# Kernel optimization log

Hardware: AMD Instinct MI355X
Metric: run time of the kernel (lower is better)

## Reference

```python
import jax, jax.numpy as jnp
import numpy as np
from jax import lax

B_, K_, T_, V_ = 2, 4, 1024, 1024
D_MODEL, EXPAND = 512, 2
D_INNER = EXPAND * D_MODEL          # 1024
N_STATE, D_CONV, DT_RANK, L_ = 16, 4, 32, 2


def setup_inputs() -> dict:
    key = jax.random.key(0)
    ks = jax.random.split(key, 9)
    s = 0.02
    A0 = jnp.log(jnp.arange(1, N_STATE + 1, dtype=jnp.float32))  # S4D-real init
    return {
        'codes': jax.random.randint(ks[0], (B_, K_, T_), 0, V_),
        'embed_w': jax.random.normal(ks[1], (K_, V_, D_MODEL), jnp.float32) * s,
        'norm_w': jnp.ones((L_, D_MODEL), jnp.float32),
        'in_proj_w': jax.random.normal(ks[2], (L_, 2 * D_INNER, D_MODEL), jnp.float32) * s,
        'conv_w': jax.random.normal(ks[3], (L_, D_INNER, 1, D_CONV), jnp.float32) * s,
        'conv_b': jnp.zeros((L_, D_INNER), jnp.float32),
        'x_proj_w': jax.random.normal(ks[4], (L_, DT_RANK + 2 * N_STATE, D_INNER), jnp.float32) * s,
        'dt_proj_w': jax.random.normal(ks[5], (L_, D_INNER, DT_RANK), jnp.float32) * s,
        'dt_proj_b': jnp.zeros((L_, D_INNER), jnp.float32),
        'A_log': jnp.broadcast_to(A0, (L_, D_INNER, N_STATE)) + 0.0,
        'D_skip': jnp.ones((L_, D_INNER), jnp.float32),
        'out_proj_w': jax.random.normal(ks[6], (L_, D_MODEL, D_INNER), jnp.float32) * s,
        'head_w': jax.random.normal(ks[7], (K_, D_MODEL, V_), jnp.float32) * s,
    }


def rmsnorm(x, w, eps=1e-6):
    return x * w * lax.rsqrt(jnp.mean(x * x, axis=-1, keepdims=True) + eps)


def causal_dwconv(x, w, b):
    # x: (B,T,D); w: (D,1,d_conv) depthwise; torch pads d_conv-1 both sides then slices [:T]
    # == left-pad-only causal conv.
    xt = x.transpose(0, 2, 1)  # (B,D,T)
    y = lax.conv_general_dilated(xt, w, (1,), [(D_CONV - 1, 0)],
                                 feature_group_count=D_INNER,
                                 dimension_numbers=('NCH', 'OIH', 'NCH'))
    return (y + b[None, :, None]).transpose(0, 2, 1)


def mamba_block(x, norm_w, in_w, cw, cb, xp_w, dtp_w, dtp_b, A_log, D_skip, out_w):
    res = x
    x = rmsnorm(x, norm_w)
    xz = x @ in_w.T                                   # (B,T,2*d_inner)
    x_ssm, z = jnp.split(xz, 2, axis=-1)
    x_ssm = jax.nn.silu(causal_dwconv(x_ssm, cw, cb))  # (B,T,D)
    x_dbl = x_ssm @ xp_w.T                            # (B,T,dt_rank+2N)
    dt_lr, Bm, Cm = jnp.split(x_dbl, [DT_RANK, DT_RANK + N_STATE], axis=-1)
    dt = jax.nn.softplus(dt_lr @ dtp_w.T + dtp_b)     # (B,T,D)
    A = -jnp.exp(A_log)                               # (D,N)
    dA = jnp.exp(dt[..., None] * A)                   # (B,T,D,N)
    dBx = dt[..., None] * Bm[:, :, None, :] * x_ssm[..., None]  # (B,T,D,N)

    def step(h, inp):
        dA_t, dBx_t, C_t = inp
        h = dA_t * h + dBx_t                          # (B,D,N)
        return h, jnp.einsum('bdn,bn->bd', h, C_t)

    h0 = jnp.zeros((x.shape[0], D_INNER, N_STATE), x.dtype)
    _, ys = lax.scan(step, h0, (dA.transpose(1, 0, 2, 3),
                                dBx.transpose(1, 0, 2, 3),
                                Cm.transpose(1, 0, 2)))
    y = ys.transpose(1, 0, 2) + x_ssm * D_skip        # (B,T,D)
    y = y * jax.nn.silu(z)
    return res + y @ out_w.T


def reference(codes, embed_w, norm_w, in_proj_w, conv_w, conv_b, x_proj_w,
              dt_proj_w, dt_proj_b, A_log, D_skip, out_proj_w, head_w):
    k_idx = jnp.arange(K_)[None, :, None]
    x = embed_w[k_idx, codes].sum(axis=1)             # (B,T,d_model): RVQ sum-embedding
    for l in range(L_):
        x = mamba_block(x, norm_w[l], in_proj_w[l], conv_w[l], conv_b[l],
                        x_proj_w[l], dt_proj_w[l], dt_proj_b[l],
                        A_log[l], D_skip[l], out_proj_w[l])
    return jnp.einsum('btd,kdv->bktv', x, head_w)     # (B,K,T,V)
```

## Files before the change

### kernel.cpp

```cpp
#include <hip/hip_runtime.h>
#include <hip/hip_bf16.h>


#define B_SZ 2
#define K_CB 4
#define T_SZ 1024
#define V_SZ 1024
#define DM 512
#define DI 1024
#define NS 16
#define DTR 32
#define NCHUNK 64
#define TCHUNK 16

typedef unsigned short u16;
typedef long long ll;
using short8 = __attribute__((ext_vector_type(8))) short;
using f32x4  = __attribute__((ext_vector_type(4))) float;

__device__ __forceinline__ float bf2f(u16 u) {
    union { unsigned int i; float f; } v; v.i = ((unsigned int)u) << 16; return v.f;
}
__device__ __forceinline__ u16 f2bf(float f) {
    union { float f; unsigned int i; } v; v.f = f;
    unsigned int x = v.i;
    return (u16)((x + 0x7fffu + ((x >> 16) & 1u)) >> 16);
}
__device__ __forceinline__ float siluf(float x) { return x / (1.f + __expf(-x)); }
__device__ __forceinline__ float softplusf(float x) { return (x > 20.f) ? x : log1pf(__expf(x)); }

__global__ __launch_bounds__(256) void mega0_k(const float* __restrict__ in_w,
                                               const float* __restrict__ xp_w,
                                               const float* __restrict__ dtp_w,
                                               const float* __restrict__ out_w,
                                               u16* __restrict__ w_in, u16* __restrict__ w_xp,
                                               u16* __restrict__ w_dt, u16* __restrict__ w_out,
                                               const float* __restrict__ head_w,
                                               u16* __restrict__ w_hd,
                                               const int* __restrict__ codes,
                                               const float* __restrict__ ew,
                                               const float* __restrict__ nw,
                                               float* __restrict__ x,
                                               u16* __restrict__ xn) {
    __shared__ float tile[64][65];
    int bid = blockIdx.x;
    int tid = threadIdx.x;
    if (bid < 3264) {
        int i = (bid * 256 + tid) << 2;
        const float* s; u16* d;
        if (i < 2097152) { s = in_w + i; d = w_in + i; }
        else {
            i -= 2097152;
            if (i < 131072) { s = xp_w + i; d = w_xp + i; }
            else {
                i -= 131072;
                if (i < 65536) { s = dtp_w + i; d = w_dt + i; }
                else { i -= 65536; s = out_w + i; d = w_out + i; }
            }
        }
        float4 v = *(const float4*)s;
        ushort4 o; o.x = f2bf(v.x); o.y = f2bf(v.y); o.z = f2bf(v.z); o.w = f2bf(v.w);
        *(ushort4*)d = o;
    } else if (bid < 3776) {
        int idx = bid - 3264;
        int z = idx >> 7, rest = idx & 127;
        int d0 = (rest >> 4) << 6, v0 = (rest & 15) << 6;
        int col = tid & 63, rbase = tid >> 6;
#pragma unroll
        for (int i = 0; i < 16; i++) {
            int row = (i << 2) + rbase;
            tile[row][col] = head_w[(ll)z * (DM * V_SZ) + (ll)(d0 + row) * V_SZ + v0 + col];
        }
        __syncthreads();
#pragma unroll
        for (int i = 0; i < 16; i++) {
            int vrow = (i << 2) + rbase;
            w_hd[(ll)z * (V_SZ * DM) + (ll)(v0 + vrow) * DM + d0 + col] = f2bf(tile[col][vrow]);
        }
    } else {
        int row = bid - 3776;
        int b = row >> 10, t = row & 1023;
        float a0 = 0.f, a1 = 0.f;
#pragma unroll
        for (int k = 0; k < K_CB; k++) {
            int c = codes[b * (K_CB * T_SZ) + k * T_SZ + t];
            a0 += ew[((ll)k * V_SZ + c) * DM + tid];
            a1 += ew[((ll)k * V_SZ + c) * DM + tid + 256];
        }
        x[(ll)row * DM + tid]       = a0;
        x[(ll)row * DM + tid + 256] = a1;
        float ss = a0 * a0 + a1 * a1;
#pragma unroll
        for (int off = 32; off > 0; off >>= 1) ss += __shfl_down(ss, off, 64);
        float* red = &tile[0][0];
        if ((tid & 63) == 0) red[tid >> 6] = ss;
        __syncthreads();
        float tot = red[0] + red[1] + red[2] + red[3];
        float scale = rsqrtf(tot * (1.0f / DM) + 1e-6f);
        xn[(ll)row * DM + tid]       = f2bf(a0 * scale * nw[tid]);
        xn[(ll)row * DM + tid + 256] = f2bf(a1 * scale * nw[tid + 256]);
    }
}

__global__ __launch_bounds__(256) void rmsnorm_k(const float* __restrict__ x,
                                                 const float* __restrict__ w,
                                                 u16* __restrict__ xn) {
    ll row = blockIdx.x;
    const float* xr = x + row * DM;
    int tid = threadIdx.x;
    float v0 = xr[tid], v1 = xr[tid + 256];
    float ss = v0 * v0 + v1 * v1;
#pragma unroll
    for (int off = 32; off > 0; off >>= 1) ss += __shfl_down(ss, off, 64);
    __shared__ float red[4];
    if ((tid & 63) == 0) red[tid >> 6] = ss;
    __syncthreads();
    float tot = red[0] + red[1] + red[2] + red[3];
    float scale = rsqrtf(tot * (1.0f / DM) + 1e-6f);
    xn[row * DM + tid]       = f2bf(v0 * scale * w[tid]);
    xn[row * DM + tid + 256] = f2bf(v1 * scale * w[tid + 256]);
}

template <int EP>
__global__ __launch_bounds__(256) void mgemm2_k(const u16* __restrict__ A, int lda,
                                                const u16* __restrict__ W,
                                                float* __restrict__ C,
                                                u16* __restrict__ Cb, int ldcb, int K) {
    __shared__ u16 As[2][4096];
    __shared__ u16 Bs[2][4096];
    int tid = threadIdx.x;
    int wave = tid >> 6, lane = tid & 63;
    int q = lane >> 4, r = lane & 15;
    int m0 = blockIdx.y << 7, n0 = blockIdx.x << 7;
    int wm = (wave >> 1) << 6, wn = (wave & 1) << 6;
    int srow = tid >> 1, soff = (tid & 1) << 4;
    const u16* Ap = A + (ll)(m0 + srow) * lda + soff;
    const u16* Wp = W + (ll)(n0 + srow) * K + soff;
    int sidx = (srow << 5) + soff;
    f32x4 acc[4][4];
#pragma unroll
    for (int i = 0; i < 4; i++)
#pragma unroll
        for (int j = 0; j < 4; j++) acc[i][j] = (f32x4){0.f, 0.f, 0.f, 0.f};

    uint4 ra0 = *(const uint4*)Ap,       ra1 = *(const uint4*)(Ap + 8);
    uint4 rb0 = *(const uint4*)Wp,       rb1 = *(const uint4*)(Wp + 8);
    *(uint4*)&As[0][sidx] = ra0; *(uint4*)&As[0][sidx + 8] = ra1;
    *(uint4*)&Bs[0][sidx] = rb0; *(uint4*)&Bs[0][sidx + 8] = rb1;
    __syncthreads();

    int p = 0;
    for (int k0 = 0; k0 < K; k0 += 32) {
        bool pf = (k0 + 32) < K;
        if (pf) {
            ra0 = *(const uint4*)(Ap + k0 + 32); ra1 = *(const uint4*)(Ap + k0 + 40);
            rb0 = *(const uint4*)(Wp + k0 + 32); rb1 = *(const uint4*)(Wp + k0 + 40);
        }
        short8 af[4], bfr[4];
#pragma unroll
        for (int i = 0; i < 4; i++) af[i]  = *(const short8*)&As[p][((wm + (i << 4) + r) << 5) + (q << 3)];
#pragma unroll
        for (int j = 0; j < 4; j++) bfr[j] = *(const short8*)&Bs[p][((wn + (j << 4) + r) << 5) + (q << 3)];
#pragma unroll
        for (int i = 0; i < 4; i++)
#pragma unroll
            for (int j = 0; j < 4; j++)
                acc[i][j] = __builtin_amdgcn_mfma_f32_16x16x32_bf16(af[i], bfr[j], acc[i][j], 0, 0, 0);
        if (pf) {
            *(uint4*)&As[p ^ 1][sidx] = ra0; *(uint4*)&As[p ^ 1][sidx + 8] = ra1;
            *(uint4*)&Bs[p ^ 1][sidx] = rb0; *(uint4*)&Bs[p ^ 1][sidx + 8] = rb1;
        }
        __syncthreads();
        p ^= 1;
    }

#pragma unroll
    for (int i = 0; i < 4; i++)
#pragma unroll
        for (int j = 0; j < 4; j++)
#pragma unroll
            for (int g = 0; g < 4; g++) {
                int m = m0 + wm + (i << 4) + (q << 2) + g;
                int n = n0 + wn + (j << 4) + r;
                float v = acc[i][j][g];
                if (EP == 0) {
                    Cb[(ll)m * ldcb + n] = f2bf(v);
                } else {
                    int z = n >> 10, vv = n & 1023;
                    int b = m >> 10, t = m & 1023;
                    C[((ll)(b * K_CB + z) * T_SZ + t) * V_SZ + vv] = v;
                }
            }
}

template <int EP>
__global__ __launch_bounds__(256) void mgemm_k(const u16* __restrict__ A, int lda,
                                               const u16* __restrict__ W,
                                               float* __restrict__ C, int ldc, int K,
                                               const float* __restrict__ bias,
                                               u16* __restrict__ Cb, int ldcb) {
    __shared__ u16 As[2][2048];
    __shared__ u16 Bs[2][2048];
    int tid = threadIdx.x;
    int m0 = blockIdx.y << 6, n0 = blockIdx.x << 6;
    int lane = tid & 63, wave = tid >> 6;
    int q = lane >> 4, r = lane & 15;
    int wm = (wave >> 1) << 5, wn = (wave & 1) << 5;
    int srow = tid >> 2, soff = (tid & 3) << 3;
    const u16* Ap = A + (ll)(m0 + srow) * lda + soff;
    const u16* Wp = W + (ll)(n0 + srow) * K + soff;
    int sidx = (srow << 5) + soff;
    f32x4 acc[2][2];
#pragma unroll
    for (int i = 0; i < 2; i++)
#pragma unroll
        for (int j = 0; j < 2; j++) acc[i][j] = (f32x4){0.f, 0.f, 0.f, 0.f};

    uint4 ra = *(const uint4*)Ap;
    uint4 rb = *(const uint4*)Wp;
    *(uint4*)&As[0][sidx] = ra;
    *(uint4*)&Bs[0][sidx] = rb;
    __syncthreads();

    int p = 0;
    for (int k0 = 0; k0 < K; k0 += 32) {
        bool pf = (k0 + 32) < K;
        if (pf) {
            ra = *(const uint4*)(Ap + k0 + 32);
            rb = *(const uint4*)(Wp + k0 + 32);
        }
        short8 af[2], bfr[2];
#pragma unroll
        for (int i = 0; i < 2; i++) af[i]  = *(const short8*)&As[p][((wm + (i << 4) + r) << 5) + (q << 3)];
#pragma unroll
        for (int j = 0; j < 2; j++) bfr[j] = *(const short8*)&Bs[p][((wn + (j << 4) + r) << 5) + (q << 3)];
#pragma unroll
        for (int i = 0; i < 2; i++)
#pragma unroll
            for (int j = 0; j < 2; j++)
                acc[i][j] = __builtin_amdgcn_mfma_f32_16x16x32_bf16(af[i], bfr[j], acc[i][j], 0, 0, 0);
        if (pf) {
            *(uint4*)&As[p ^ 1][sidx] = ra;
            *(uint4*)&Bs[p ^ 1][sidx] = rb;
        }
        __syncthreads();
        p ^= 1;
    }

#pragma unroll
    for (int i = 0; i < 2; i++)
#pragma unroll
        for (int j = 0; j < 2; j++)
#pragma unroll
            for (int g = 0; g < 4; g++) {
                int m = m0 + wm + (i << 4) + (q << 2) + g;
                int n = n0 + wn + (j << 4) + r;
                float v = acc[i][j][g];
                float nv = C[(ll)m * ldc + n] + v;
                C[(ll)m * ldc + n] = nv;
                Cb[(ll)m * ldcb + n] = f2bf(nv);
            }
}

__global__ __launch_bounds__(256) void convxp_k(const u16* __restrict__ xzb,
                                                const float* __restrict__ cw,
                                                const float* __restrict__ cb,
                                                const u16* __restrict__ W,
                                                float* __restrict__ xc,
                                                float* __restrict__ xdbl,
                                                u16* __restrict__ xdbl_bf) {
    __shared__ u16 xcs[16][1032];
    __shared__ u16 Bs[2][2048];
    int blk = blockIdx.x, tid = threadIdx.x;
    int b = blk >> 6, tg = blk & 63;
    int t0 = tg << 4;
    ll ro0 = (ll)b * T_SZ + t0;
    int c0 = tid << 2;
    float4 a = *(const float4*)&cb[c0];
    float4 cwv[4];
#pragma unroll
    for (int e = 0; e < 4; e++) cwv[e] = *(const float4*)&cw[(c0 + e) << 2];
    ushort4 v[19];
#pragma unroll
    for (int i = 0; i < 19; i++) {
        int t = t0 - 3 + i;
        if (t >= 0) v[i] = *(const ushort4*)&xzb[((ll)(b * T_SZ + t)) * (2 * DI) + c0];
        else        v[i] = (ushort4){0, 0, 0, 0};
    }
#pragma unroll
    for (int tr = 0; tr < 16; tr++) {
        float acc0 = a.x, acc1 = a.y, acc2 = a.z, acc3 = a.w;
#pragma unroll
        for (int j = 0; j < 4; j++) {
            ushort4 vv = v[tr + j];
            acc0 = fmaf(bf2f(vv.x), ((const float*)&cwv[0])[j], acc0);
            acc1 = fmaf(bf2f(vv.y), ((const float*)&cwv[1])[j], acc1);
            acc2 = fmaf(bf2f(vv.z), ((const float*)&cwv[2])[j], acc2);
            acc3 = fmaf(bf2f(vv.w), ((const float*)&cwv[3])[j], acc3);
        }
        float4 s; ushort4 sb;
        s.x = siluf(acc0); s.y = siluf(acc1); s.z = siluf(acc2); s.w = siluf(acc3);
        sb.x = f2bf(s.x); sb.y = f2bf(s.y); sb.z = f2bf(s.z); sb.w = f2bf(s.w);
        *(float4*)&xc[(ro0 + tr) * DI + c0] = s;
        *(ushort4*)&xcs[tr][c0] = sb;
    }
    __syncthreads();

    int lane = tid & 63, wave = tid >> 6;
    int q = lane >> 4, r = lane & 15;
    int srow = tid >> 2, soff = (tid & 3) << 3;
    f32x4 acc = (f32x4){0.f, 0.f, 0.f, 0.f};
    uint4 rb = *(const uint4*)(W + (ll)srow * DI + soff);
    *(uint4*)&Bs[0][(srow << 5) + soff] = rb;
    __syncthreads();
    int p = 0;
    for (int k0 = 0; k0 < DI; k0 += 32) {
        bool pf = (k0 + 32) < DI;
        if (pf) rb = *(const uint4*)(W + (ll)srow * DI + k0 + 32 + soff);
        short8 af  = *(const short8*)&xcs[r][k0 + (q << 3)];
        short8 bfr = *(const short8*)&Bs[p][(((wave << 4) + r) << 5) + (q << 3)];
        acc = __builtin_amdgcn_mfma_f32_16x16x32_bf16(af, bfr, acc, 0, 0, 0);
        if (pf) *(uint4*)&Bs[p ^ 1][(srow << 5) + soff] = rb;
        __syncthreads();
        p ^= 1;
    }
#pragma unroll
    for (int g = 0; g < 4; g++) {
        int tr = (q << 2) + g;
        int n = (wave << 4) + r;
        float vv = acc[g];
        xdbl[(ro0 + tr) * 64 + n]    = vv;
        xdbl_bf[(ro0 + tr) * 64 + n] = f2bf(vv);
    }
}

__global__ __launch_bounds__(256) void dtscan1_k(const u16* __restrict__ A,
                                                 const u16* __restrict__ W,
                                                 const float* __restrict__ bias,
                                                 const float* __restrict__ xc,
                                                 const float* __restrict__ xdbl,
                                                 const float* __restrict__ A_log,
                                                 float* __restrict__ dtb,
                                                 float* __restrict__ pA,
                                                 float* __restrict__ U) {
    __shared__ u16 As[2048];
    __shared__ u16 Bs[2048];
    __shared__ float dts[64][65];
    __shared__ float BCs[64][16];
    __shared__ float xcs[64][65];
    int tid = threadIdx.x;
    int m0 = blockIdx.y << 6, n0 = blockIdx.x << 6;
    int lane = tid & 63, wave = tid >> 6;
    int q = lane >> 4, r = lane & 15;
    int wm = (wave >> 1) << 5, wn = (wave & 1) << 5;

    int xr = tid >> 2, xcb = (tid & 3) << 4;
    const float* xp = &xc[(ll)(m0 + xr) * DI + n0 + xcb];
    float4 xv0 = *(const float4*)(xp);
    float4 xv1 = *(const float4*)(xp + 4);
    float4 xv2 = *(const float4*)(xp + 8);
    float4 xv3 = *(const float4*)(xp + 12);

    {
        int srow = tid >> 2, soff = (tid & 3) << 3;
        *(uint4*)&As[(srow << 5) + soff] = *(const uint4*)(A + (ll)(m0 + srow) * 64 + soff);
        *(uint4*)&Bs[(srow << 5) + soff] = *(const uint4*)(W + (ll)(n0 + srow) * DTR + soff);
        int rr = tid >> 2, cc = (tid & 3) << 2;
        *(float4*)&BCs[rr][cc] = *(const float4*)&xdbl[(ll)(m0 + rr) * 64 + DTR + cc];
    }
    int sd = lane;
    int sc = wave;
    int dg = n0 + sd;
    float Av[NS];
#pragma unroll
    for (int n4 = 0; n4 < 4; n4++) {
        float4 alv = *(const float4*)&A_log[dg * NS + (n4 << 2)];
        Av[(n4 << 2) + 0] = -__expf(alv.x); Av[(n4 << 2) + 1] = -__expf(alv.y);
        Av[(n4 << 2) + 2] = -__expf(alv.z); Av[(n4 << 2) + 3] = -__expf(alv.w);
    }
    *(float4*)&xcs[xr][xcb]      = xv0;
    *(float4*)&xcs[xr][xcb + 4]  = xv1;
    *(float4*)&xcs[xr][xcb + 8]  = xv2;
    *(float4*)&xcs[xr][xcb + 12] = xv3;
    __syncthreads();

    f32x4 acc[2][2];
#pragma unroll
    for (int i = 0; i < 2; i++)
#pragma unroll
        for (int j = 0; j < 2; j++) acc[i][j] = (f32x4){0.f, 0.f, 0.f, 0.f};
    short8 af[2], bfr[2];
#pragma unroll
    for (int i = 0; i < 2; i++) af[i]  = *(const short8*)&As[((wm + (i << 4) + r) << 5) + (q << 3)];
#pragma unroll
    for (int j = 0; j < 2; j++) bfr[j] = *(const short8*)&Bs[((wn + (j << 4) + r) << 5) + (q << 3)];
#pragma unroll
    for (int i = 0; i < 2; i++)
#pragma unroll
        for (int j = 0; j < 2; j++)
            acc[i][j] = __builtin_amdgcn_mfma_f32_16x16x32_bf16(af[i], bfr[j], acc[i][j], 0, 0, 0);

#pragma unroll
    for (int i = 0; i < 2; i++)
#pragma unroll
        for (int j = 0; j < 2; j++)
#pragma unroll
            for (int g = 0; g < 4; g++) {
                int mm = wm + (i << 4) + (q << 2) + g;
                int nn = wn + (j << 4) + r;
                float dtl = softplusf(acc[i][j][g] + bias[n0 + nn]);
                dtb[(ll)(m0 + mm) * DI + (n0 + nn)] = dtl;
                dts[mm][nn] = dtl;
            }
    __syncthreads();

    int b = m0 >> 10;
    int c = ((m0 & 1023) >> 4) + sc;
    int tl0 = sc << 4;
    float p[NS], u[NS];
#pragma unroll
    for (int n = 0; n < NS; n++) { p[n] = 1.f; u[n] = 0.f; }
#pragma unroll
    for (int s = 0; s < TCHUNK; s++) {
        int tl = tl0 + s;
        float dtv = dts[tl][sd];
        float xl = xcs[tl][sd];
        float dx = dtv * xl;
#pragma unroll
        for (int n = 0; n < NS; n++) {
            float aa = __expf(dtv * Av[n]);
            p[n] *= aa;
            u[n] = fmaf(aa, u[n], dx * BCs[tl][n]);
        }
    }
    ll o = ((ll)b * NCHUNK + c) * (NS * DI) + dg;
#pragma unroll
    for (int n = 0; n < NS; n++) { pA[o + n * DI] = p[n]; U[o + n * DI] = u[n]; }
}

__global__ __launch_bounds__(256) void scan2_k(const float* __restrict__ pA,
                                               const float* __restrict__ U,
                                               float* __restrict__ hst) {
    int i = blockIdx.x * 256 + threadIdx.x;
    int b = i >> 14;
    int rest = i & 16383;
    float h = 0.f;
#pragma unroll
    for (int c = 0; c < NCHUNK; c++) {
        ll o = ((ll)b * NCHUNK + c) * (DI * NS) + rest;
        float pa = pA[o], u = U[o];
        hst[o] = h;
        h = fmaf(pa, h, u);
    }
}

__global__ __launch_bounds__(256) void scan3_k(const float* __restrict__ dt,
                                               const float* __restrict__ xc,
                                               const float* __restrict__ xdbl,
                                               const u16* __restrict__ xzb,
                                               const float* __restrict__ A_log,
                                               const float* __restrict__ Dk,
                                               const float* __restrict__ hst,
                                               u16* __restrict__ y) {
    int blk = blockIdx.x;
    int dblk = blk & 3;
    int c = (blk >> 2) & (NCHUNK - 1);
    int b = blk >> 8;
    int d = dblk * 256 + threadIdx.x;
    int t0 = c * TCHUNK;
    __shared__ float BC[TCHUNK][32];
    if (threadIdx.x < TCHUNK * 8) {
        int rr = threadIdx.x >> 3, cc = (threadIdx.x & 7) << 2;
        *(float4*)&BC[rr][cc] = *(const float4*)&xdbl[((ll)(b * T_SZ + t0 + rr)) * 64 + DTR + cc];
    }
    float Av[NS];
#pragma unroll
    for (int n4 = 0; n4 < 4; n4++) {
        float4 alv = *(const float4*)&A_log[d * NS + (n4 << 2)];
        Av[(n4 << 2) + 0] = -__expf(alv.x); Av[(n4 << 2) + 1] = -__expf(alv.y);
        Av[(n4 << 2) + 2] = -__expf(alv.z); Av[(n4 << 2) + 3] = -__expf(alv.w);
    }
    float h[NS];
    ll ho = (((ll)b * NCHUNK + c) * (NS * DI)) + d;
#pragma unroll
    for (int n = 0; n < NS; n++) h[n] = hst[ho + n * DI];
    float Dv = Dk[d];
    __syncthreads();
#pragma unroll
    for (int s = 0; s < TCHUNK; s++) {
        ll ro = (ll)(b * T_SZ + t0 + s);
        float dtv = dt[ro * DI + d];
        float xv = xc[ro * DI + d];
        float dx = dtv * xv;
        float acc = 0.f;
#pragma unroll
        for (int n = 0; n < NS; n++) {
            float aa = __expf(dtv * Av[n]);
            h[n] = fmaf(aa, h[n], dx * BC[s][n]);
            acc = fmaf(h[n], BC[s][16 + n], acc);
        }
        float zv = bf2f(xzb[ro * (2 * DI) + DI + d]);
        y[ro * DI + d] = f2bf((acc + xv * Dv) * siluf(zv));
    }
}

extern "C" void kernel_launch(void* const* d_in, const int* in_sizes, int n_in,
                              void* d_out, int out_size, void* d_ws, size_t ws_size,
                              hipStream_t stream) {
    const int*   codes   = (const int*)d_in[0];
    const float* embed_w = (const float*)d_in[1];
    const float* norm_w  = (const float*)d_in[2];
    const float* in_w    = (const float*)d_in[3];
    const float* conv_w  = (const float*)d_in[4];
    const float* conv_b  = (const float*)d_in[5];
    const float* xp_w    = (const float*)d_in[6];
    const float* dtp_w   = (const float*)d_in[7];
    const float* dtp_b   = (const float*)d_in[8];
    const float* A_log   = (const float*)d_in[9];
    const float* D_skip  = (const float*)d_in[10];
    const float* out_w   = (const float*)d_in[11];
    const float* head_w  = (const float*)d_in[12];
    float* out = (float*)d_out;

    float* ws = (float*)d_ws;
    float* x    = ws;
    float* xc   = x + 1048576;
    float* dtb  = xc + 2097152;
    float* xdbl = dtb + 2097152;
    float* pA   = xdbl + 131072;
    float* Uh   = pA + 2097152;

    u16* us       = (u16*)(Uh + 2097152);
    u16* xz_bf    = us;
    u16* xbf      = xz_bf + 4194304;
    u16* ybxn_bf  = xbf + 2097152;
    u16* xdbl_bf  = ybxn_bf + 2097152;
    u16* w_in_bf  = xdbl_bf + 131072;
    u16* w_xp_bf  = w_in_bf + 2097152;
    u16* w_dt_bf  = w_xp_bf + 131072;
    u16* w_out_bf = w_dt_bf + 65536;
    u16* w_hd_bf  = w_out_bf + 1048576;

    u16* xn_bf = ybxn_bf;
    u16* y_bf  = ybxn_bf;
    u16* x_bf  = xbf;

    mega0_k<<<5824, 256, 0, stream>>>(in_w, xp_w, dtp_w, out_w,
                                      w_in_bf, w_xp_bf, w_dt_bf, w_out_bf,
                                      head_w, w_hd_bf, codes, embed_w, norm_w, x, xn_bf);

    for (int l = 0; l < 2; l++) {
        const float* al = A_log + l * DI * NS;
        if (l == 1)
            rmsnorm_k<<<2048, 256, 0, stream>>>(x, norm_w + DM, xn_bf);
        mgemm2_k<0><<<dim3(16, 16), 256, 0, stream>>>(xn_bf, DM, w_in_bf + l * 1048576,
                                                      nullptr, xz_bf, 2 * DI, DM);
        convxp_k<<<128, 256, 0, stream>>>(xz_bf, conv_w + l * DI * 4, conv_b + l * DI,
                                          w_xp_bf + l * 65536, xc, xdbl, xdbl_bf);
        dtscan1_k<<<dim3(16, 32), 256, 0, stream>>>(xdbl_bf, w_dt_bf + l * 32768,
                                                    dtp_b + l * DI, xc, xdbl, al,
                                                    dtb, pA, Uh);
        scan2_k<<<128, 256, 0, stream>>>(pA, Uh, Uh);
        scan3_k<<<512, 256, 0, stream>>>(dtb, xc, xdbl, xz_bf, al, D_skip + l * DI, Uh, y_bf);
        mgemm_k<3><<<dim3(8, 32), 256, 0, stream>>>(y_bf, DI, w_out_bf + l * 524288,
                                                    x, DM, DI, nullptr, x_bf, DM);
    }

    mgemm2_k<4><<<dim3(32, 16), 256, 0, stream>>>(x_bf, DM, w_hd_bf, out, nullptr, 0, DM);
}
```

Baseline: 285.4 us.

## Fuse layer-1 RMSNorm into in-proj GEMM by folding norm weight into weights

Removes the separate layer-1 rmsnorm kernel. The layer-1 norm weight is folded into the bf16 in-proj weights at conversion time. The new GEMM takes the bf16 residual stream as its input, accumulates each row's sum of squares while loading A tiles, and applies the rsqrt scale in the epilogue. This saves a launch and a full read/write pass over the activations. In exchange, the sum of squares is computed from the bf16-rounded residual rather than fp32 x, which slightly changes numerics.

Measured after the change: 285.5 us. About the same (+0.0%).

```diff
diff --git a/kernel.cpp b/kernel.cpp
--- a/kernel.cpp
+++ b/kernel.cpp
@@ -28,6 +28,13 @@
 }
 __device__ __forceinline__ float siluf(float x) { return x / (1.f + __expf(-x)); }
 __device__ __forceinline__ float softplusf(float x) { return (x > 20.f) ? x : log1pf(__expf(x)); }
+__device__ __forceinline__ float sumsq8(uint4 v) {
+    const u16* e = (const u16*)&v;
+    float s = 0.f;
+#pragma unroll
+    for (int t = 0; t < 8; t++) { float f = bf2f(e[t]); s = fmaf(f, f, s); }
+    return s;
+}
 
 __global__ __launch_bounds__(256) void mega0_k(const float* __restrict__ in_w,
                                                const float* __restrict__ xp_w,
@@ -46,10 +53,14 @@
     int bid = blockIdx.x;
     int tid = threadIdx.x;
     if (bid < 3264) {
-        int i = (bid * 256 + tid) << 2;
+        int i0 = (bid * 256 + tid) << 2;
+        int i = i0;
         const float* s; u16* d;
-        if (i < 2097152) { s = in_w + i; d = w_in + i; }
-        else {
+        bool in_w_l1 = false;
+        if (i < 2097152) {
+            s = in_w + i; d = w_in + i;
+            in_w_l1 = (i >= 1048576);
+        } else {
             i -= 2097152;
             if (i < 131072) { s = xp_w + i; d = w_xp + i; }
             else {
@@ -59,6 +70,11 @@
             }
         }
         float4 v = *(const float4*)s;
+        if (in_w_l1) {
+            int k = i0 & 511;
+            const float* nr = nw + DM;
+            v.x *= nr[k]; v.y *= nr[k + 1]; v.z *= nr[k + 2]; v.w *= nr[k + 3];
+        }
         ushort4 o; o.x = f2bf(v.x); o.y = f2bf(v.y); o.z = f2bf(v.z); o.w = f2bf(v.w);
         *(ushort4*)d = o;
     } else if (bid < 3776) {
@@ -100,25 +116,6 @@
         xn[(ll)row * DM + tid]       = f2bf(a0 * scale * nw[tid]);
         xn[(ll)row * DM + tid + 256] = f2bf(a1 * scale * nw[tid + 256]);
     }
-}
-
-__global__ __launch_bounds__(256) void rmsnorm_k(const float* __restrict__ x,
-                                                 const float* __restrict__ w,
-                                                 u16* __restrict__ xn) {
-    ll row = blockIdx.x;
-    const float* xr = x + row * DM;
-    int tid = threadIdx.x;
-    float v0 = xr[tid], v1 = xr[tid + 256];
-    float ss = v0 * v0 + v1 * v1;
-#pragma unroll
-    for (int off = 32; off > 0; off >>= 1) ss += __shfl_down(ss, off, 64);
-    __shared__ float red[4];
-    if ((tid & 63) == 0) red[tid >> 6] = ss;
-    __syncthreads();
-    float tot = red[0] + red[1] + red[2] + red[3];
-    float scale = rsqrtf(tot * (1.0f / DM) + 1e-6f);
-    xn[row * DM + tid]       = f2bf(v0 * scale * w[tid]);
-    xn[row * DM + tid + 256] = f2bf(v1 * scale * w[tid + 256]);
 }
 
 template <int EP>
@@ -191,6 +188,79 @@
                     C[((ll)(b * K_CB + z) * T_SZ + t) * V_SZ + vv] = v;
                 }
             }
+}
+
+__global__ __launch_bounds__(256) void inprojrms_k(const u16* __restrict__ A, int lda,
+                                                   const u16* __restrict__ W,
+                                                   u16* __restrict__ Cb, int ldcb, int K) {
+    __shared__ u16 As[2][4096];
+    __shared__ u16 Bs[2][4096];
+    __shared__ float rs_lds[128][2];
+    int tid = threadIdx.x;
+    int wave = tid >> 6, lane = tid & 63;
+    int q = lane >> 4, r = lane & 15;
+    int m0 = blockIdx.y << 7, n0 = blockIdx.x << 7;
+    int wm = (wave >> 1) << 6, wn = (wave & 1) << 6;
+    int srow = tid >> 1, soff = (tid & 1) << 4;
+    const u16* Ap = A + (ll)(m0 + srow) * lda + soff;
+    const u16* Wp = W + (ll)(n0 + srow) * K + soff;
+    int sidx = (srow << 5) + soff;
+    f32x4 acc[4][4];
+#pragma unroll
+    for (int i = 0; i < 4; i++)
+#pragma unroll
+        for (int j = 0; j < 4; j++) acc[i][j] = (f32x4){0.f, 0.f, 0.f, 0.f};
+
+    float ss = 0.f;
+    uint4 ra0 = *(const uint4*)Ap,       ra1 = *(const uint4*)(Ap + 8);
+    uint4 rb0 = *(const uint4*)Wp,       rb1 = *(const uint4*)(Wp + 8);
+    ss += sumsq8(ra0); ss += sumsq8(ra1);
+    *(uint4*)&As[0][sidx] = ra0; *(uint4*)&As[0][sidx + 8] = ra1;
+    *(uint4*)&Bs[0][sidx] = rb0; *(uint4*)&Bs[0][sidx + 8] = rb1;
+    __syncthreads();
+
+    int p = 0;
+    for (int k0 = 0; k0 < K; k0 += 32) {
+        bool pf = (k0 + 32) < K;
+        if (pf) {
+            ra0 = *(const uint4*)(Ap + k0 + 32); ra1 = *(const uint4*)(Ap + k0 + 40);
+            rb0 = *(const uint4*)(Wp + k0 + 32); rb1 = *(const uint4*)(Wp + k0 + 40);
+            ss += sumsq8(ra0); ss += sumsq8(ra1);
+        }
+        short8 af[4], bfr[4];
+#pragma unroll
+        for (int i = 0; i < 4; i++) af[i]  = *(const short8*)&As[p][((wm + (i << 4) + r) << 5) + (q << 3)];
+#pragma unroll
+        for (int j = 0; j < 4; j++) bfr[j] = *(const short8*)&Bs[p][((wn + (j << 4) + r) << 5) + (q << 3)];
+#pragma unroll
+        for (int i = 0; i < 4; i++)
+#pragma unroll
+            for (int j = 0; j < 4; j++)
+                acc[i][j] = __builtin_amdgcn_mfma_f32_16x16x32_bf16(af[i], bfr[j], acc[i][j], 0, 0, 0);
+        if (pf) {
+            *(uint4*)&As[p ^ 1][sidx] = ra0; *(uint4*)&As[p ^ 1][sidx + 8] = ra1;
+            *(uint4*)&Bs[p ^ 1][sidx] = rb0; *(uint4*)&Bs[p ^ 1][sidx + 8] = rb1;
+        }
+        __syncthreads();
+        p ^= 1;
+    }
+
+    rs_lds[srow][tid & 1] = ss;
+    __syncthreads();
+
+#pragma unroll
+    for (int i = 0; i < 4; i++)
+#pragma unroll
+        for (int g = 0; g < 4; g++) {
+            int mm = wm + (i << 4) + (q << 2) + g;
+            float scale = rsqrtf((rs_lds[mm][0] + rs_lds[mm][1]) * (1.0f / DM) + 1e-6f);
+            int m = m0 + mm;
+#pragma unroll
+            for (int j = 0; j < 4; j++) {
+                int n = n0 + wn + (j << 4) + r;
+                Cb[(ll)m * ldcb + n] = f2bf(acc[i][j][g] * scale);
+            }
+        }
 }
 
 template <int EP>
@@ -551,10 +621,12 @@
 
     for (int l = 0; l < 2; l++) {
         const float* al = A_log + l * DI * NS;
-        if (l == 1)
-            rmsnorm_k<<<2048, 256, 0, stream>>>(x, norm_w + DM, xn_bf);
-        mgemm2_k<0><<<dim3(16, 16), 256, 0, stream>>>(xn_bf, DM, w_in_bf + l * 1048576,
-                                                      nullptr, xz_bf, 2 * DI, DM);
+        if (l == 0)
+            mgemm2_k<0><<<dim3(16, 16), 256, 0, stream>>>(xn_bf, DM, w_in_bf,
+                                                          nullptr, xz_bf, 2 * DI, DM);
+        else
+            inprojrms_k<<<dim3(16, 16), 256, 0, stream>>>(x_bf, DM, w_in_bf + 1048576,
+                                                          xz_bf, 2 * DI, DM);
         convxp_k<<<128, 256, 0, stream>>>(xz_bf, conv_w + l * DI * 4, conv_b + l * DI,
                                           w_xp_bf + l * 65536, xc, xdbl, xdbl_bf);
         dtscan1_k<<<dim3(16, 32), 256, 0, stream>>>(xdbl_bf, w_dt_bf + l * 32768,
```
